# Optimization experiments

Hardware: AMD Instinct MI355X
Metric: run time of the kernel (lower is better)

## Reference

```python
import jax, jax.numpy as jnp
import numpy as np
import math

B, S, D, H = 2, 2048, 1024, 16
HD = D // H  # 64


def setup_inputs() -> dict:
    key = jax.random.key(0)
    ks = jax.random.split(key, 10)
    s = 1.0 / math.sqrt(D)
    return {
        "q": jax.random.normal(ks[0], (B, S, D), jnp.float32),
        "k": jax.random.normal(ks[1], (B, S, D), jnp.float32),
        "v": jax.random.normal(ks[2], (B, S, D), jnp.float32),
        "attention_mask": jnp.zeros((B, 1, 1, S), jnp.float32),
        "Wq": jax.random.normal(ks[3], (D, D), jnp.float32) * s,
        "bq": jnp.zeros((D,), jnp.float32),
        "Wk": jax.random.normal(ks[4], (D, D), jnp.float32) * s,
        "bk": jnp.zeros((D,), jnp.float32),
        "Wv": jax.random.normal(ks[5], (D, D), jnp.float32) * s,
        "bv": jnp.zeros((D,), jnp.float32),
    }


def reference(q, k, v, attention_mask, Wq, bq, Wk, bk, Wv, bv):
    # QKV projections (torch Linear: x @ W^T + b)
    def split_heads(x):  # [B,S,D] -> [B,H,S,HD]
        return x.reshape(B, S, H, HD).transpose(0, 2, 1, 3)

    ql = split_heads(q @ Wq.T + bq)
    kl = split_heads(k @ Wk.T + bk)
    vl = split_heads(v @ Wv.T + bv)

    scale = 1.0 / math.sqrt(HD)
    scores = jnp.einsum("bhqd,bhkd->bhqk", ql, kl) * scale + attention_mask
    probs = jax.nn.softmax(scores, axis=-1)  # dropout prob = 0.0 -> identity
    ctx = jnp.einsum("bhqk,bhkd->bhqd", probs, vl)
    ctx = ctx.transpose(0, 2, 1, 3).reshape(B, S, D)
    return ctx, scores
```

## Files before the change

kernel.cpp:

```cpp
#include <hip/hip_runtime.h>

typedef __bf16 bf16;
typedef __bf16 bf16x4 __attribute__((ext_vector_type(4)));
typedef __bf16 bf16x8 __attribute__((ext_vector_type(8)));
typedef float f32x4 __attribute__((ext_vector_type(4)));

#define LOG2E 1.4426950408889634f

__global__ __launch_bounds__(256, 2)
void proj_kernel(const float* __restrict__ Xq, const float* __restrict__ Xk,
                 const float* __restrict__ Xv,
                 const float* __restrict__ Wq, const float* __restrict__ Wk,
                 const float* __restrict__ Wv,
                 const float* __restrict__ Bq, const float* __restrict__ Bk,
                 const float* __restrict__ Bv,
                 bf16* __restrict__ Oq, bf16* __restrict__ Ok,
                 bf16* __restrict__ Ov)
{
    const int z = blockIdx.z;
    const float* X  = (z == 0) ? Xq : (z == 1) ? Xk : Xv;
    const float* W  = (z == 0) ? Wq : (z == 1) ? Wk : Wv;
    const float* Bi = (z == 0) ? Bq : (z == 1) ? Bk : Bv;

    const int n0 = blockIdx.x * 128;
    const int m0 = blockIdx.y * 128;

    __shared__ bf16 As[128 * 40];
    __shared__ bf16 Bs[128 * 40];

    const int t = threadIdx.x;
    const int w = t >> 6, l = t & 63, quad = l >> 4, ln = l & 15;
    const int wm = (w & 1) * 64, wn = (w >> 1) * 64;

    const f32x4 zero4 = {0.f, 0.f, 0.f, 0.f};
    f32x4 acc[4][4];
    for (int mi = 0; mi < 4; mi++)
        for (int ni = 0; ni < 4; ni++) acc[mi][ni] = zero4;

    for (int k0 = 0; k0 < 1024; k0 += 32) {
        for (int i = 0; i < 4; i++) {
            int idx = i * 256 + t;
            int row = idx >> 3, c4 = idx & 7;
            float4 a  = *(const float4*)&X[(size_t)(m0 + row) * 1024 + k0 + c4 * 4];
            float4 bb = *(const float4*)&W[(size_t)(n0 + row) * 1024 + k0 + c4 * 4];
            bf16x4 av, bv;
            av[0] = (bf16)a.x;  av[1] = (bf16)a.y;  av[2] = (bf16)a.z;  av[3] = (bf16)a.w;
            bv[0] = (bf16)bb.x; bv[1] = (bf16)bb.y; bv[2] = (bf16)bb.z; bv[3] = (bf16)bb.w;
            *(bf16x4*)&As[row * 40 + c4 * 4] = av;
            *(bf16x4*)&Bs[row * 40 + c4 * 4] = bv;
        }
        __syncthreads();

        bf16x8 af[4], bfv[4];
        for (int mi = 0; mi < 4; mi++)
            af[mi] = *(const bf16x8*)&As[(wm + mi * 16 + ln) * 40 + quad * 8];
        for (int ni = 0; ni < 4; ni++)
            bfv[ni] = *(const bf16x8*)&Bs[(wn + ni * 16 + ln) * 40 + quad * 8];
        for (int mi = 0; mi < 4; mi++)
            for (int ni = 0; ni < 4; ni++)
                acc[mi][ni] = __builtin_amdgcn_mfma_f32_16x16x32_bf16(
                    af[mi], bfv[ni], acc[mi][ni], 0, 0, 0);
        __syncthreads();
    }

    bf16* Onat = (z == 0) ? Oq : Ok;
    for (int ni = 0; ni < 4; ni++) {
        int n = n0 + wn + ni * 16 + ln;
        float bias = Bi[n];
        for (int mi = 0; mi < 4; mi++) {
            int mbase = m0 + wm + mi * 16 + quad * 4;
            if (z < 2) {
                for (int r = 0; r < 4; r++)
                    Onat[(size_t)(mbase + r) * 1024 + n] = (bf16)(acc[mi][ni][r] + bias);
            } else {
                int b = mbase >> 11, s0 = mbase & 2047;
                bf16x4 vv;
                for (int r = 0; r < 4; r++) vv[r] = (bf16)(acc[mi][ni][r] + bias);
                *(bf16x4*)&Ov[(size_t)(b * 1024 + n) * 2048 + s0] = vv;
            }
        }
    }
}

__global__ __launch_bounds__(256, 2)
void attn_kernel(const bf16* __restrict__ Qp, const bf16* __restrict__ Kp,
                 const bf16* __restrict__ Vt, const float* __restrict__ mask,
                 float* __restrict__ ctx, float* __restrict__ scores)
{
    const int qt = blockIdx.x, h = blockIdx.y, b = blockIdx.z;
    const int q0 = qt * 128;
    const int t = threadIdx.x, w = t >> 6, l = t & 63, quad = l >> 4, ln = l & 15;

    __shared__ bf16 Qs[128 * 72];
    __shared__ bf16 Ks[64 * 72];
    __shared__ bf16 VTs[64 * 72];
    __shared__ bf16 Ps[128 * 72];

    for (int i = 0; i < 4; i++) {
        int idx = i * 256 + t;
        int row = idx >> 3, d8 = idx & 7;
        *(bf16x8*)&Qs[row * 72 + d8 * 8] =
            *(const bf16x8*)&Qp[(size_t)(b * 2048 + q0 + row) * 1024 + h * 64 + d8 * 8];
    }
    __syncthreads();

    bf16x8 aq[2][2];
    for (int mi = 0; mi < 2; mi++)
        for (int ks = 0; ks < 2; ks++)
            aq[mi][ks] = *(const bf16x8*)&Qs[(w * 32 + mi * 16 + ln) * 72 + ks * 32 + quad * 8];

    const f32x4 zero4 = {0.f, 0.f, 0.f, 0.f};
    f32x4 O[2][4];
    for (int mi = 0; mi < 2; mi++)
        for (int ni = 0; ni < 4; ni++) O[mi][ni] = zero4;
    float mst[2][4], lst[2][4];
    for (int mi = 0; mi < 2; mi++)
        for (int r = 0; r < 4; r++) { mst[mi][r] = -1e30f; lst[mi][r] = 0.f; }

    const int srow_base = (b * 16 + h) * 2048 + q0 + w * 32;

    for (int kt = 0; kt < 32; kt++) {
        const int kk0 = kt * 64;
        __syncthreads();
        for (int i = 0; i < 2; i++) {
            int idx = i * 256 + t;
            int row = idx >> 3, d8 = idx & 7;
            *(bf16x8*)&Ks[row * 72 + d8 * 8] =
                *(const bf16x8*)&Kp[(size_t)(b * 2048 + kk0 + row) * 1024 + h * 64 + d8 * 8];
            *(bf16x8*)&VTs[row * 72 + d8 * 8] =
                *(const bf16x8*)&Vt[(size_t)(b * 1024 + h * 64 + row) * 2048 + kk0 + d8 * 8];
        }
        __syncthreads();

        f32x4 sa[2][4];
        for (int mi = 0; mi < 2; mi++)
            for (int ni = 0; ni < 4; ni++) sa[mi][ni] = zero4;
        for (int ks = 0; ks < 2; ks++) {
            bf16x8 kf[4];
            for (int ni = 0; ni < 4; ni++)
                kf[ni] = *(const bf16x8*)&Ks[(ni * 16 + ln) * 72 + ks * 32 + quad * 8];
            for (int mi = 0; mi < 2; mi++)
                for (int ni = 0; ni < 4; ni++)
                    sa[mi][ni] = __builtin_amdgcn_mfma_f32_16x16x32_bf16(
                        aq[mi][ks], kf[ni], sa[mi][ni], 0, 0, 0);
        }

        float maskv[4];
        for (int ni = 0; ni < 4; ni++)
            maskv[ni] = mask[b * 2048 + kk0 + ni * 16 + ln];

        float rmax[2][4];
        for (int mi = 0; mi < 2; mi++)
            for (int r = 0; r < 4; r++) rmax[mi][r] = -1e30f;
        for (int mi = 0; mi < 2; mi++) {
            for (int ni = 0; ni < 4; ni++) {
                int col = kk0 + ni * 16 + ln;
                for (int r = 0; r < 4; r++) {
                    float v = sa[mi][ni][r] * 0.125f + maskv[ni];
                    sa[mi][ni][r] = v;
                    scores[(size_t)(srow_base + mi * 16 + quad * 4 + r) * 2048 + col] = v;
                    rmax[mi][r] = fmaxf(rmax[mi][r], v);
                }
            }
        }
        for (int mi = 0; mi < 2; mi++)
            for (int r = 0; r < 4; r++) {
                float v = rmax[mi][r];
                v = fmaxf(v, __shfl_xor(v, 1));
                v = fmaxf(v, __shfl_xor(v, 2));
                v = fmaxf(v, __shfl_xor(v, 4));
                v = fmaxf(v, __shfl_xor(v, 8));
                rmax[mi][r] = v;
            }

        float alpha[2][4];
        for (int mi = 0; mi < 2; mi++)
            for (int r = 0; r < 4; r++) {
                float mnew = fmaxf(mst[mi][r], rmax[mi][r]);
                alpha[mi][r] = exp2f((mst[mi][r] - mnew) * LOG2E);
                mst[mi][r] = mnew;
            }

        float rsum[2][4];
        for (int mi = 0; mi < 2; mi++)
            for (int r = 0; r < 4; r++) rsum[mi][r] = 0.f;
        for (int mi = 0; mi < 2; mi++)
            for (int ni = 0; ni < 4; ni++)
                for (int r = 0; r < 4; r++) {
                    float p = exp2f((sa[mi][ni][r] - mst[mi][r]) * LOG2E);
                    rsum[mi][r] += p;
                    Ps[(w * 32 + mi * 16 + quad * 4 + r) * 72 + ni * 16 + ln] = (bf16)p;
                }
        for (int mi = 0; mi < 2; mi++)
            for (int r = 0; r < 4; r++) {
                float v = rsum[mi][r];
                v += __shfl_xor(v, 1);
                v += __shfl_xor(v, 2);
                v += __shfl_xor(v, 4);
                v += __shfl_xor(v, 8);
                lst[mi][r] = lst[mi][r] * alpha[mi][r] + v;
            }

        for (int mi = 0; mi < 2; mi++)
            for (int ni = 0; ni < 4; ni++)
                for (int r = 0; r < 4; r++) O[mi][ni][r] *= alpha[mi][r];

        for (int ks = 0; ks < 2; ks++) {
            bf16x8 pf[2], vf[4];
            for (int mi = 0; mi < 2; mi++)
                pf[mi] = *(const bf16x8*)&Ps[(w * 32 + mi * 16 + ln) * 72 + ks * 32 + quad * 8];
            for (int ni = 0; ni < 4; ni++)
                vf[ni] = *(const bf16x8*)&VTs[(ni * 16 + ln) * 72 + ks * 32 + quad * 8];
            for (int mi = 0; mi < 2; mi++)
                for (int ni = 0; ni < 4; ni++)
                    O[mi][ni] = __builtin_amdgcn_mfma_f32_16x16x32_bf16(
                        pf[mi], vf[ni], O[mi][ni], 0, 0, 0);
        }
    }

    for (int mi = 0; mi < 2; mi++)
        for (int ni = 0; ni < 4; ni++) {
            int n = h * 64 + ni * 16 + ln;
            for (int r = 0; r < 4; r++) {
                int row = b * 2048 + q0 + w * 32 + mi * 16 + quad * 4 + r;
                ctx[(size_t)row * 1024 + n] = O[mi][ni][r] / lst[mi][r];
            }
        }
}

extern "C" void kernel_launch(void* const* d_in, const int* in_sizes, int n_in,
                              void* d_out, int out_size, void* d_ws, size_t ws_size,
                              hipStream_t stream) {
    const float* q    = (const float*)d_in[0];
    const float* k    = (const float*)d_in[1];
    const float* v    = (const float*)d_in[2];
    const float* mask = (const float*)d_in[3];
    const float* Wq   = (const float*)d_in[4];
    const float* bq   = (const float*)d_in[5];
    const float* Wk   = (const float*)d_in[6];
    const float* bk   = (const float*)d_in[7];
    const float* Wv   = (const float*)d_in[8];
    const float* bv   = (const float*)d_in[9];

    bf16* Qp = (bf16*)d_ws;
    bf16* Kp = Qp + (size_t)4096 * 1024;
    bf16* Vt = Kp + (size_t)4096 * 1024;

    float* ctx    = (float*)d_out;
    float* scores = ctx + (size_t)2 * 2048 * 1024;

    proj_kernel<<<dim3(8, 32, 3), 256, 0, stream>>>(
        q, k, v, Wq, Wk, Wv, bq, bk, bv, Qp, Kp, Vt);
    attn_kernel<<<dim3(16, 16, 2), 256, 0, stream>>>(
        Qp, Kp, Vt, mask, ctx, scores);
}
```

Baseline: 737.8 us.

## Transpose attention MFMA operands for vectorized score stores and XCD-aware block remap

Swaps the MFMA operand order (K·Q and V·P) so each lane holds four consecutive key columns of one query row. This enables 16-byte nontemporal stores of the fp32 scores matrix, vectorized mask loads, and vectorized ctx stores, and it cuts the softmax row reductions to two cross-lane shuffles. The grid is also flattened to 1D with a block-index remap intended to spread work across the chiplets for L2 locality of K/V. Ps is now written with bf16x4 stores, which may introduce LDS bank conflicts.

New measurement: 737.6 us. No clear change (-0.0%).

```diff
diff --git a/kernel.cpp b/kernel.cpp
--- a/kernel.cpp
+++ b/kernel.cpp
@@ -87,7 +87,10 @@
                  const bf16* __restrict__ Vt, const float* __restrict__ mask,
                  float* __restrict__ ctx, float* __restrict__ scores)
 {
-    const int qt = blockIdx.x, h = blockIdx.y, b = blockIdx.z;
+    const int lid = blockIdx.x;
+    const int wg  = (lid & 7) * 64 + (lid >> 3);
+    const int qt = wg & 15, h = (wg >> 4) & 15, b = wg >> 8;
+
     const int q0 = qt * 128;
     const int t = threadIdx.x, w = t >> 6, l = t & 63, quad = l >> 4, ln = l & 15;
 
@@ -104,20 +107,21 @@
     }
     __syncthreads();
 
-    bf16x8 aq[2][2];
+    bf16x8 qf[2][2];
+#pragma unroll
     for (int mi = 0; mi < 2; mi++)
+#pragma unroll
         for (int ks = 0; ks < 2; ks++)
-            aq[mi][ks] = *(const bf16x8*)&Qs[(w * 32 + mi * 16 + ln) * 72 + ks * 32 + quad * 8];
+            qf[mi][ks] = *(const bf16x8*)&Qs[(w * 32 + mi * 16 + ln) * 72 + ks * 32 + quad * 8];
 
     const f32x4 zero4 = {0.f, 0.f, 0.f, 0.f};
-    f32x4 O[2][4];
-    for (int mi = 0; mi < 2; mi++)
-        for (int ni = 0; ni < 4; ni++) O[mi][ni] = zero4;
-    float mst[2][4], lst[2][4];
-    for (int mi = 0; mi < 2; mi++)
-        for (int r = 0; r < 4; r++) { mst[mi][r] = -1e30f; lst[mi][r] = 0.f; }
-
-    const int srow_base = (b * 16 + h) * 2048 + q0 + w * 32;
+    f32x4 Ot[4][2];
+#pragma unroll
+    for (int ni = 0; ni < 4; ni++)
+#pragma unroll
+        for (int mi = 0; mi < 2; mi++) Ot[ni][mi] = zero4;
+    float mst[2] = {-1e30f, -1e30f};
+    float lst[2] = {0.f, 0.f};
 
     for (int kt = 0; kt < 32; kt++) {
         const int kk0 = kt * 64;
@@ -132,100 +136,110 @@
         }
         __syncthreads();
 
-        f32x4 sa[2][4];
-        for (int mi = 0; mi < 2; mi++)
-            for (int ni = 0; ni < 4; ni++) sa[mi][ni] = zero4;
+        f32x4 st[4][2];
+#pragma unroll
+        for (int ni = 0; ni < 4; ni++)
+#pragma unroll
+            for (int mi = 0; mi < 2; mi++) st[ni][mi] = zero4;
+#pragma unroll
         for (int ks = 0; ks < 2; ks++) {
             bf16x8 kf[4];
+#pragma unroll
             for (int ni = 0; ni < 4; ni++)
                 kf[ni] = *(const bf16x8*)&Ks[(ni * 16 + ln) * 72 + ks * 32 + quad * 8];
-            for (int mi = 0; mi < 2; mi++)
-                for (int ni = 0; ni < 4; ni++)
-                    sa[mi][ni] = __builtin_amdgcn_mfma_f32_16x16x32_bf16(
-                        aq[mi][ks], kf[ni], sa[mi][ni], 0, 0, 0);
-        }
-
-        float maskv[4];
+#pragma unroll
+            for (int ni = 0; ni < 4; ni++)
+#pragma unroll
+                for (int mi = 0; mi < 2; mi++)
+                    st[ni][mi] = __builtin_amdgcn_mfma_f32_16x16x32_bf16(
+                        kf[ni], qf[mi][ks], st[ni][mi], 0, 0, 0);
+        }
+
+        f32x4 mv[4];
+#pragma unroll
         for (int ni = 0; ni < 4; ni++)
-            maskv[ni] = mask[b * 2048 + kk0 + ni * 16 + ln];
-
-        float rmax[2][4];
-        for (int mi = 0; mi < 2; mi++)
-            for (int r = 0; r < 4; r++) rmax[mi][r] = -1e30f;
+            mv[ni] = *(const f32x4*)&mask[b * 2048 + kk0 + ni * 16 + quad * 4];
+
+#pragma unroll
         for (int mi = 0; mi < 2; mi++) {
+            const size_t srow =
+                ((size_t)((b * 16 + h) * 2048 + q0 + w * 32 + mi * 16 + ln)) * 2048 + kk0;
+#pragma unroll
             for (int ni = 0; ni < 4; ni++) {
-                int col = kk0 + ni * 16 + ln;
+                f32x4 v = st[ni][mi];
+#pragma unroll
+                for (int r = 0; r < 4; r++) v[r] = v[r] * 0.125f + mv[ni][r];
+                st[ni][mi] = v;
+                __builtin_nontemporal_store(
+                    v, (f32x4*)&scores[srow + ni * 16 + quad * 4]);
+            }
+        }
+
+#pragma unroll
+        for (int mi = 0; mi < 2; mi++) {
+            float rm = -1e30f;
+#pragma unroll
+            for (int ni = 0; ni < 4; ni++)
+#pragma unroll
+                for (int r = 0; r < 4; r++) rm = fmaxf(rm, st[ni][mi][r]);
+            rm = fmaxf(rm, __shfl_xor(rm, 16));
+            rm = fmaxf(rm, __shfl_xor(rm, 32));
+            const float mnew  = fmaxf(mst[mi], rm);
+            const float alpha = exp2f((mst[mi] - mnew) * LOG2E);
+            mst[mi] = mnew;
+
+            float rs = 0.f;
+#pragma unroll
+            for (int ni = 0; ni < 4; ni++) {
+                bf16x4 pv;
+#pragma unroll
                 for (int r = 0; r < 4; r++) {
-                    float v = sa[mi][ni][r] * 0.125f + maskv[ni];
-                    sa[mi][ni][r] = v;
-                    scores[(size_t)(srow_base + mi * 16 + quad * 4 + r) * 2048 + col] = v;
-                    rmax[mi][r] = fmaxf(rmax[mi][r], v);
+                    float p = exp2f((st[ni][mi][r] - mnew) * LOG2E);
+                    rs += p;
+                    pv[r] = (bf16)p;
                 }
+                *(bf16x4*)&Ps[(w * 32 + mi * 16 + ln) * 72 + ni * 16 + quad * 4] = pv;
             }
-        }
-        for (int mi = 0; mi < 2; mi++)
-            for (int r = 0; r < 4; r++) {
-                float v = rmax[mi][r];
-                v = fmaxf(v, __shfl_xor(v, 1));
-                v = fmaxf(v, __shfl_xor(v, 2));
-                v = fmaxf(v, __shfl_xor(v, 4));
-                v = fmaxf(v, __shfl_xor(v, 8));
-                rmax[mi][r] = v;
-            }
-
-        float alpha[2][4];
-        for (int mi = 0; mi < 2; mi++)
-            for (int r = 0; r < 4; r++) {
-                float mnew = fmaxf(mst[mi][r], rmax[mi][r]);
-                alpha[mi][r] = exp2f((mst[mi][r] - mnew) * LOG2E);
-                mst[mi][r] = mnew;
-            }
-
-        float rsum[2][4];
-        for (int mi = 0; mi < 2; mi++)
-            for (int r = 0; r < 4; r++) rsum[mi][r] = 0.f;
-        for (int mi = 0; mi < 2; mi++)
-            for (int ni = 0; ni < 4; ni++)
-                for (int r = 0; r < 4; r++) {
-                    float p = exp2f((sa[mi][ni][r] - mst[mi][r]) * LOG2E);
-                    rsum[mi][r] += p;
-                    Ps[(w * 32 + mi * 16 + quad * 4 + r) * 72 + ni * 16 + ln] = (bf16)p;
-                }
-        for (int mi = 0; mi < 2; mi++)
-            for (int r = 0; r < 4; r++) {
-                float v = rsum[mi][r];
-                v += __shfl_xor(v, 1);
-                v += __shfl_xor(v, 2);
-                v += __shfl_xor(v, 4);
-                v += __shfl_xor(v, 8);
-                lst[mi][r] = lst[mi][r] * alpha[mi][r] + v;
-            }
-
-        for (int mi = 0; mi < 2; mi++)
-            for (int ni = 0; ni < 4; ni++)
-                for (int r = 0; r < 4; r++) O[mi][ni][r] *= alpha[mi][r];
-
+            rs += __shfl_xor(rs, 16);
+            rs += __shfl_xor(rs, 32);
+            lst[mi] = lst[mi] * alpha + rs;
+
+#pragma unroll
+            for (int ni = 0; ni < 4; ni++)
+#pragma unroll
+                for (int r = 0; r < 4; r++) Ot[ni][mi][r] *= alpha;
+        }
+
+#pragma unroll
         for (int ks = 0; ks < 2; ks++) {
-            bf16x8 pf[2], vf[4];
+            bf16x8 vf[4], pf[2];
+#pragma unroll
+            for (int ni = 0; ni < 4; ni++)
+                vf[ni] = *(const bf16x8*)&VTs[(ni * 16 + ln) * 72 + ks * 32 + quad * 8];
+#pragma unroll
             for (int mi = 0; mi < 2; mi++)
                 pf[mi] = *(const bf16x8*)&Ps[(w * 32 + mi * 16 + ln) * 72 + ks * 32 + quad * 8];
-            for (int ni = 0; ni < 4; ni++)
-                vf[ni] = *(const bf16x8*)&VTs[(ni * 16 + ln) * 72 + ks * 32 + quad * 8];
-            for (int mi = 0; mi < 2; mi++)
-                for (int ni = 0; ni < 4; ni++)
-                    O[mi][ni] = __builtin_amdgcn_mfma_f32_16x16x32_bf16(
-                        pf[mi], vf[ni], O[mi][ni], 0, 0, 0);
-        }
-    }
-
-    for (int mi = 0; mi < 2; mi++)
+#pragma unroll
+            for (int ni = 0; ni < 4; ni++)
+#pragma unroll
+                for (int mi = 0; mi < 2; mi++)
+                    Ot[ni][mi] = __builtin_amdgcn_mfma_f32_16x16x32_bf16(
+                        vf[ni], pf[mi], Ot[ni][mi], 0, 0, 0);
+        }
+    }
+
+#pragma unroll
+    for (int mi = 0; mi < 2; mi++) {
+        const float rl = 1.0f / lst[mi];
+        const int row = b * 2048 + q0 + w * 32 + mi * 16 + ln;
+#pragma unroll
         for (int ni = 0; ni < 4; ni++) {
-            int n = h * 64 + ni * 16 + ln;
-            for (int r = 0; r < 4; r++) {
-                int row = b * 2048 + q0 + w * 32 + mi * 16 + quad * 4 + r;
-                ctx[(size_t)row * 1024 + n] = O[mi][ni][r] / lst[mi][r];
-            }
-        }
+            f32x4 o = Ot[ni][mi];
+#pragma unroll
+            for (int r = 0; r < 4; r++) o[r] *= rl;
+            *(f32x4*)&ctx[(size_t)row * 1024 + h * 64 + ni * 16 + quad * 4] = o;
+        }
+    }
 }
 
 extern "C" void kernel_launch(void* const* d_in, const int* in_sizes, int n_in,
@@ -251,6 +265,6 @@
 
     proj_kernel<<<dim3(8, 32, 3), 256, 0, stream>>>(
         q, k, v, Wq, Wk, Wv, bq, bk, bv, Qp, Kp, Vt);
-    attn_kernel<<<dim3(16, 16, 2), 256, 0, stream>>>(
+    attn_kernel<<<dim3(512, 1, 1), 256, 0, stream>>>(
         Qp, Kp, Vt, mask, ctx, scores);
 }
```
